# Optimization experiments

Measured on AMD Instinct MI355X. Metric: run time of the kernel, lower is better.

Reference implementation:

```python
import jax, jax.numpy as jnp
import numpy as np

N_H, N_O, D = 5000, 15000, 1024
E_HH, E_OO, E_HO = 20000, 40000, 40000


def setup_inputs() -> dict:
    key = jax.random.key(0)
    ks = jax.random.split(key, 20)
    N = N_H + N_O
    w = lambda k, shp: jax.random.normal(k, shp, dtype=jnp.float32) * 0.02
    inp = {
        'n_f': jax.random.normal(ks[0], (N, D), dtype=jnp.float32),
        'src_hh': jax.random.randint(ks[1], (E_HH,), 0, N_H),
        'dst_hh': jax.random.randint(ks[2], (E_HH,), 0, N_H),
        'src_oo': jax.random.randint(ks[3], (E_OO,), 0, N_O) + N_H,
        'dst_oo': jax.random.randint(ks[4], (E_OO,), 0, N_O) + N_H,
        'src_ho': jax.random.randint(ks[5], (E_HO,), 0, N_H),
        'dst_ho': jax.random.randint(ks[6], (E_HO,), 0, N_O) + N_H,
        'W_hh': w(ks[7], (2 * D, D)), 'b_hh': jnp.zeros((D,), jnp.float32),
        'W_oo': w(ks[8], (2 * D, D)), 'b_oo': jnp.zeros((D,), jnp.float32),
        'W_ho': w(ks[9], (2 * D, D)), 'b_ho': jnp.zeros((D,), jnp.float32),
        'W_att': w(ks[10], (D, 1)), 'b_att': jnp.zeros((1,), jnp.float32),
        'W_hn': w(ks[11], (2 * D, D)), 'b_hn': jnp.zeros((D,), jnp.float32),
        'W_on': w(ks[12], (2 * D, D)), 'b_on': jnp.zeros((D,), jnp.float32),
    }
    return inp


def reference(n_f, src_hh, dst_hh, src_oo, dst_oo, src_ho, dst_ho,
              W_hh, b_hh, W_oo, b_oo, W_ho, b_ho, W_att, b_att,
              W_hn, b_hn, W_on, b_on):
    N = n_f.shape[0]

    def edge_mlp(src, dst, W, b):
        # gather -> concat -> Linear -> ReLU  (H_H/O_O/H_O EdgeApplyModule)
        feat = jnp.concatenate([n_f[src], n_f[dst]], axis=1)  # [E, 2D]
        return jax.nn.relu(feat @ W + b)                       # [E, D]

    e_f = jnp.concatenate([
        edge_mlp(src_hh, dst_hh, W_hh, b_hh),
        edge_mlp(src_oo, dst_oo, W_oo, b_oo),
        edge_mlp(src_ho, dst_ho, W_ho, b_ho),
    ], axis=0)                                                 # [E, D]
    src = jnp.concatenate([src_hh, src_oo, src_ho])
    dst = jnp.concatenate([dst_hh, dst_oo, dst_ho])

    # E_AttentionModule: per-edge scalar attention logit
    a = (e_f @ W_att + b_att)[:, 0]                            # [E]

    # update_all: per-destination softmax over incoming edges (mailbox softmax)
    seg_max = jax.ops.segment_max(a, dst, num_segments=N)
    seg_max = jnp.where(jnp.isfinite(seg_max), seg_max, 0.0)
    ex = jnp.exp(a - seg_max[dst])
    denom = jax.ops.segment_sum(ex, dst, num_segments=N)
    alpha = ex / jnp.where(denom[dst] == 0, 1.0, denom[dst])   # [E]
    z = jax.ops.segment_sum(alpha[:, None] * n_f[src], dst, num_segments=N)  # [N, D]

    # Node apply: concat(n_f, z_f) -> Linear -> ReLU, separate h/o MLPs
    new_h = jax.nn.relu(jnp.concatenate([n_f[:N_H], z[:N_H]], axis=1) @ W_hn + b_hn)
    new_o = jax.nn.relu(jnp.concatenate([n_f[N_H:], z[N_H:]], axis=1) @ W_on + b_on)
    return jnp.concatenate([new_h, new_o], axis=0)             # [N, D] new_n_f
```

## Files before the change

kernel.cpp:

```cpp
#include <hip/hip_runtime.h>

#define N_H   5000
#define N_O   15000
#define N_TOT 20000
#define DD    1024
#define E_HH  20000
#define E_OO  40000
#define E_HO  40000
#define E_TOT 100000

typedef unsigned short u16;
typedef unsigned int u32;
typedef __attribute__((ext_vector_type(8))) short short8;
typedef __attribute__((ext_vector_type(4))) float f32x4;
typedef const __attribute__((address_space(1))) u32 gas_u32;
typedef __attribute__((address_space(3))) u32 las_u32;

__device__ __forceinline__ float bf2f(u16 u) {
    union { unsigned int i; float f; } v; v.i = ((unsigned int)u) << 16; return v.f;
}
__device__ __forceinline__ u16 f2bf(float f) {
    union { float f; unsigned int i; } v; v.f = f;
    unsigned int u = v.i;
    return (u16)((u + 0x7FFFu + ((u >> 16) & 1u)) >> 16);
}

#define CAST_NB 10000
#define CAT_NB  391
#define TW_NB   10240
struct TW  { const float* W; u16* dT; u16* dB; int ld; };
struct TW5 { TW t[5]; };
__global__ void cast_cat_tw(const float* __restrict__ in, u16* __restrict__ out,
                            const int* __restrict__ shh, const int* __restrict__ dhh,
                            const int* __restrict__ soo, const int* __restrict__ doo,
                            const int* __restrict__ sho, const int* __restrict__ dho,
                            int* __restrict__ src_all, int* __restrict__ dst_all,
                            int* __restrict__ deg, TW5 p) {
    __shared__ float tile[32][33];
    int b = blockIdx.x;
    if (b < CAST_NB) {
        size_t i = ((size_t)b * 256 + threadIdx.x) * 8;
        float4 a = *(const float4*)(in + i);
        float4 c = *(const float4*)(in + i + 4);
        u16 o[8] = {f2bf(a.x), f2bf(a.y), f2bf(a.z), f2bf(a.w),
                    f2bf(c.x), f2bf(c.y), f2bf(c.z), f2bf(c.w)};
        *(uint4*)(out + i) = *(const uint4*)o;
        return;
    }
    if (b < CAST_NB + CAT_NB) {
        int e = (b - CAST_NB) * 256 + threadIdx.x;
        if (e >= E_TOT) return;
        int s, d;
        if (e < E_HH)              { s = shh[e];               d = dhh[e]; }
        else if (e < E_HH + E_OO)  { s = soo[e - E_HH];        d = doo[e - E_HH]; }
        else                       { s = sho[e - E_HH - E_OO]; d = dho[e - E_HH - E_OO]; }
        src_all[e] = s; dst_all[e] = d;
        atomicAdd(&deg[d], 1);
        return;
    }
    int tb = b - CAST_NB - CAT_NB;
    int z = tb >> 10;
    int rem = tb & 1023;
    int bk = rem & 31, bn = rem >> 5;
    TW tw = p.t[z >> 1];
    int half = z & 1;
    int tx = threadIdx.x & 31, ty = threadIdx.x >> 5;
#pragma unroll
    for (int yy = 0; yy < 4; yy++) {
        int k = half * 1024 + bk * 32 + ty + yy * 8;
        int n = bn * 32 + tx;
        tile[ty + yy * 8][tx] = tw.W[(size_t)k * 1024 + n];
    }
    __syncthreads();
    u16* dst = half ? tw.dB : tw.dT;
#pragma unroll
    for (int yy = 0; yy < 4; yy++) {
        int n = bn * 32 + ty + yy * 8;
        int k = bk * 32 + tx;
        dst[(size_t)n * tw.ld + k] = f2bf(tile[tx][ty + yy * 8]);
    }
}

#define PROJ_NBM_H 40
#define PROJ_NBM_O 118
#define PROJ_NBN   24
__launch_bounds__(256)
__global__ void gemm_proj(const u16* __restrict__ Ah, const u16* __restrict__ Ao,
                          const u16* __restrict__ Bth, const u16* __restrict__ Bto,
                          u16* __restrict__ Ch, u16* __restrict__ Co) {
    __shared__ u16 smem[2][128][64];
    int bid = blockIdx.x;
    const u16* A; const u16* Bt; u16* C; int M;
    if (bid < PROJ_NBM_H * PROJ_NBN) { A = Ah; Bt = Bth; C = Ch; M = N_H; }
    else { bid -= PROJ_NBM_H * PROJ_NBN; A = Ao; Bt = Bto; C = Co; M = N_O; }
    int bm = bid / PROJ_NBN, bn = bid % PROJ_NBN;
    int t = threadIdx.x;
    int wave = t >> 6, lane = t & 63;
    int wr = wave >> 1, wc = wave & 1;
    int lm = lane & 15, q = lane >> 4;
    f32x4 acc[4][4] = {};
    int srow = lane >> 3;
    int scol = ((lane & 7) ^ srow) * 8;

    for (int k0 = 0; k0 < 1024; k0 += 64) {
#pragma unroll
        for (int it = 0; it < 4; it++) {
            int chunk = wave * 4 + it;
            int row = chunk * 8 + srow;
            int gr = bm * 128 + row; if (gr >= M) gr = M - 1;
            __builtin_amdgcn_global_load_lds((gas_u32*)(A + (size_t)gr * 1024 + k0 + scol),
                                             (las_u32*)&smem[0][chunk * 8][0], 16, 0, 0);
            __builtin_amdgcn_global_load_lds((gas_u32*)(Bt + (size_t)(bn * 128 + row) * 1024 + k0 + scol),
                                             (las_u32*)&smem[1][chunk * 8][0], 16, 0, 0);
        }
        __syncthreads();
#pragma unroll
        for (int ks = 0; ks < 64; ks += 32) {
            short8 af[4], bfr[4];
            int pc = (((ks >> 3) + q) ^ (lm & 7)) * 8;
#pragma unroll
            for (int i = 0; i < 4; i++)
                af[i] = *(const short8*)&smem[0][wr * 64 + i * 16 + lm][pc];
#pragma unroll
            for (int j = 0; j < 4; j++)
                bfr[j] = *(const short8*)&smem[1][wc * 64 + j * 16 + lm][pc];
#pragma unroll
            for (int i = 0; i < 4; i++)
#pragma unroll
                for (int j = 0; j < 4; j++)
                    acc[i][j] = __builtin_amdgcn_mfma_f32_16x16x32_bf16(af[i], bfr[j], acc[i][j], 0, 0, 0);
        }
        __syncthreads();
    }
    u16* sc = &smem[0][0][0];
#pragma unroll
    for (int i = 0; i < 4; i++)
#pragma unroll
        for (int j = 0; j < 4; j++)
#pragma unroll
            for (int r = 0; r < 4; r++)
                sc[(wr * 64 + i * 16 + q * 4 + r) * 128 + (wc * 64 + j * 16 + lm)] =
                    f2bf(acc[i][j][r]);
    __syncthreads();
#pragma unroll
    for (int it = 0; it < 8; it++) {
        int flat = it * 256 + t;
        int r = flat >> 4, cs = (flat & 15) * 8;
        int grow = bm * 128 + r;
        if (grow < M)
            *(uint4*)&C[(size_t)grow * 3072 + bn * 128 + cs] = *(const uint4*)&sc[r * 128 + cs];
    }
}

#define NODE_NBM_H 40
#define NODE_NBM_O 118
#define NODE_NBN   8
__launch_bounds__(256)
__global__ void gemm_node(const u16* __restrict__ nf_h, const u16* __restrict__ nf_o,
                          const u16* __restrict__ z_h, const u16* __restrict__ z_o,
                          const u16* __restrict__ Bthn, const u16* __restrict__ Bton,
                          const float* __restrict__ b_hn, const float* __restrict__ b_on,
                          float* __restrict__ out_h, float* __restrict__ out_o) {
    __shared__ u16 smem[2][128][64];
    int bid = (blockIdx.x & 7) * ((NODE_NBM_H + NODE_NBM_O) * NODE_NBN / 8)
            + (blockIdx.x >> 3);
    const u16 *A0, *A1, *Bt; const float* bias; float* C; int M;
    if (bid < NODE_NBM_H * NODE_NBN) {
        A0 = nf_h; A1 = z_h; Bt = Bthn; bias = b_hn; C = out_h; M = N_H;
    } else {
        bid -= NODE_NBM_H * NODE_NBN;
        A0 = nf_o; A1 = z_o; Bt = Bton; bias = b_on; C = out_o; M = N_O;
    }
    int bm = bid / NODE_NBN, bn = bid % NODE_NBN;
    int t = threadIdx.x;
    int wave = t >> 6, lane = t & 63;
    int wr = wave >> 1, wc = wave & 1;
    int lm = lane & 15, q = lane >> 4;
    f32x4 acc[4][4] = {};
    int srow = lane >> 3;
    int scol = ((lane & 7) ^ srow) * 8;

    for (int half = 0; half < 2; half++) {
        const u16* Asrc = half ? A1 : A0;
        const u16* Bth = Bt + half * 1024;
        for (int k0 = 0; k0 < 1024; k0 += 64) {
#pragma unroll
            for (int it = 0; it < 4; it++) {
                int chunk = wave * 4 + it;
                int row = chunk * 8 + srow;
                int gr = bm * 128 + row; if (gr >= M) gr = M - 1;
                __builtin_amdgcn_global_load_lds((gas_u32*)(Asrc + (size_t)gr * 1024 + k0 + scol),
                                                 (las_u32*)&smem[0][chunk * 8][0], 16, 0, 0);
                __builtin_amdgcn_global_load_lds((gas_u32*)(Bth + (size_t)(bn * 128 + row) * 2048 + k0 + scol),
                                                 (las_u32*)&smem[1][chunk * 8][0], 16, 0, 0);
            }
            __syncthreads();
#pragma unroll
            for (int ks = 0; ks < 64; ks += 32) {
                short8 af[4], bfr[4];
                int pc = (((ks >> 3) + q) ^ (lm & 7)) * 8;
#pragma unroll
                for (int i = 0; i < 4; i++)
                    af[i] = *(const short8*)&smem[0][wr * 64 + i * 16 + lm][pc];
#pragma unroll
                for (int j = 0; j < 4; j++)
                    bfr[j] = *(const short8*)&smem[1][wc * 64 + j * 16 + lm][pc];
#pragma unroll
                for (int i = 0; i < 4; i++)
#pragma unroll
                    for (int j = 0; j < 4; j++)
                        acc[i][j] = __builtin_amdgcn_mfma_f32_16x16x32_bf16(af[i], bfr[j], acc[i][j], 0, 0, 0);
            }
            __syncthreads();
        }
    }
    float* sf = (float*)&smem[0][0][0];
#pragma unroll
    for (int p = 0; p < 2; p++) {
        if (p) __syncthreads();
        if (wr == p) {
#pragma unroll
            for (int j = 0; j < 4; j++) {
                int col = wc * 64 + j * 16 + lm;
                float bv = bias[bn * 128 + col];
#pragma unroll
                for (int i = 0; i < 4; i++)
#pragma unroll
                    for (int r = 0; r < 4; r++)
                        sf[(i * 16 + q * 4 + r) * 128 + col] =
                            fmaxf(acc[i][j][r] + bv, 0.0f);
            }
        }
        __syncthreads();
#pragma unroll
        for (int it = 0; it < 8; it++) {
            int c = it * 256 + t;
            int rl = c >> 5, k4 = c & 31;
            int grow = bm * 128 + p * 64 + rl;
            if (grow < M)
                *(float4*)&C[(size_t)grow * 1024 + bn * 128 + k4 * 4] =
                    *(const float4*)&sf[rl * 128 + k4 * 4];
        }
    }
}

__global__ void edge_att(const u16* __restrict__ proj_h, const u16* __restrict__ proj_o,
                         const float* __restrict__ b_hh, const float* __restrict__ b_oo,
                         const float* __restrict__ b_ho,
                         const float* __restrict__ W_att, const float* __restrict__ b_att,
                         const int* __restrict__ src_all, const int* __restrict__ dst_all,
                         float* __restrict__ a_out) {
    int wave = threadIdx.x >> 6, lane = threadIdx.x & 63;
    int e0 = blockIdx.x * 64 + wave * 16;
    if (e0 >= E_TOT) return;
    const float* bsel = (e0 < E_HH) ? b_hh : (e0 < E_HH + E_OO ? b_oo : b_ho);
    float ww[16], bb[16];
#pragma unroll
    for (int i = 0; i < 16; i++) { ww[i] = W_att[lane * 16 + i]; bb[i] = bsel[lane * 16 + i]; }
    float batt = b_att[0];
    for (int k = 0; k < 16; k++) {
        int e = e0 + k;
        int s = src_all[e], d = dst_all[e];
        const u16 *u, *v;
        if (e < E_HH) {
            u = proj_h + (size_t)s * 3072;
            v = proj_h + (size_t)d * 3072 + 1024;
        } else if (e < E_HH + E_OO) {
            u = proj_o + (size_t)(s - N_H) * 3072;
            v = proj_o + (size_t)(d - N_H) * 3072 + 1024;
        } else {
            u = proj_h + (size_t)s * 3072 + 2048;
            v = proj_o + (size_t)(d - N_H) * 3072 + 2048;
        }
        int off = lane * 16;
        uint4 u0 = *(const uint4*)(u + off), u1 = *(const uint4*)(u + off + 8);
        uint4 v0 = *(const uint4*)(v + off), v1 = *(const uint4*)(v + off + 8);
        const u16* pu0 = (const u16*)&u0; const u16* pu1 = (const u16*)&u1;
        const u16* pv0 = (const u16*)&v0; const u16* pv1 = (const u16*)&v1;
        float acc = 0.f;
#pragma unroll
        for (int i = 0; i < 8; i++) {
            float tv = bf2f(pu0[i]) + bf2f(pv0[i]) + bb[i];
            acc += fmaxf(tv, 0.f) * ww[i];
        }
#pragma unroll
        for (int i = 0; i < 8; i++) {
            float tv = bf2f(pu1[i]) + bf2f(pv1[i]) + bb[8 + i];
            acc += fmaxf(tv, 0.f) * ww[8 + i];
        }
#pragma unroll
        for (int o = 32; o > 0; o >>= 1) acc += __shfl_down(acc, o);
        if (lane == 0) a_out[e] = acc + batt;
    }
}

__global__ void scan_deg(const int* __restrict__ deg, int* __restrict__ indptr) {
    __shared__ int sums[1024];
    int t = threadIdx.x;
    const int CH = 20;
    int beg = t * CH, end = beg + CH;
    if (end > N_TOT) end = N_TOT;
    if (beg > N_TOT) beg = N_TOT;
    int s = 0;
    for (int i = beg; i < end; i++) s += deg[i];
    sums[t] = s;
    __syncthreads();
    for (int off = 1; off < 1024; off <<= 1) {
        int v = sums[t];
        int add = (t >= off) ? sums[t - off] : 0;
        __syncthreads();
        sums[t] = v + add;
        __syncthreads();
    }
    int run = (t == 0) ? 0 : sums[t - 1];
    for (int i = beg; i < end; i++) { indptr[i] = run; run += deg[i]; }
    if (t == 1023) indptr[N_TOT] = sums[1023];
}

__global__ void fill_csr(const int* __restrict__ dst_all, const int* __restrict__ indptr,
                         int* __restrict__ cursor, int* __restrict__ edge_ids) {
    int e = blockIdx.x * 256 + threadIdx.x;
    if (e < E_TOT) {
        int d = dst_all[e];
        int pos = atomicAdd(&cursor[d], 1);
        edge_ids[indptr[d] + pos] = e;
    }
}

__launch_bounds__(256)
__global__ void soft_z_w(const float* __restrict__ a, const int* __restrict__ indptr,
                         const int* __restrict__ edge_ids, const int* __restrict__ src_all,
                         const u16* __restrict__ nf, u16* __restrict__ z) {
    int wave = threadIdx.x >> 6, lane = threadIdx.x & 63;
    int node = blockIdx.x * 4 + wave;
    if (node >= N_TOT) return;
    int beg = indptr[node];
    int deg = indptr[node + 1] - beg;
    float m = -1e30f, ssum = 0.f;
    for (int i = lane; i < deg; i += 64) {
        float av = a[edge_ids[beg + i]];
        if (av > m) { ssum *= __expf(m - av); m = av; }
        ssum += __expf(av - m);
    }
#pragma unroll
    for (int o = 32; o > 0; o >>= 1) {
        float m2 = __shfl_xor(m, o);
        float s2 = __shfl_xor(ssum, o);
        float mn = fmaxf(m, m2);
        ssum = ssum * __expf(m - mn) + s2 * __expf(m2 - mn);
        m = mn;
    }
    float inv = (ssum > 0.f) ? 1.0f / ssum : 0.f;
    float av16[16] = {};
    int base = lane * 16;
    for (int i = 0; i < deg; i++) {
        int eid = edge_ids[beg + i];
        float al = __expf(a[eid] - m) * inv;
        const u16* row = nf + (size_t)src_all[eid] * DD + base;
        uint4 p0 = *(const uint4*)row;
        uint4 p1 = *(const uint4*)(row + 8);
        const u16* pp0 = (const u16*)&p0;
        const u16* pp1 = (const u16*)&p1;
#pragma unroll
        for (int j = 0; j < 8; j++) av16[j]     += al * bf2f(pp0[j]);
#pragma unroll
        for (int j = 0; j < 8; j++) av16[8 + j] += al * bf2f(pp1[j]);
    }
    u16 ov[16];
#pragma unroll
    for (int j = 0; j < 16; j++) ov[j] = f2bf(av16[j]);
    const uint4* po = (const uint4*)ov;
    *(uint4*)(z + (size_t)node * DD + base)     = po[0];
    *(uint4*)(z + (size_t)node * DD + base + 8) = po[1];
}

extern "C" void kernel_launch(void* const* d_in, const int* in_sizes, int n_in,
                              void* d_out, int out_size, void* d_ws, size_t ws_size,
                              hipStream_t stream) {
    const float* nf   = (const float*)d_in[0];
    const int* shh    = (const int*)d_in[1];
    const int* dhh    = (const int*)d_in[2];
    const int* soo    = (const int*)d_in[3];
    const int* doo    = (const int*)d_in[4];
    const int* sho    = (const int*)d_in[5];
    const int* dho    = (const int*)d_in[6];
    const float* W_hh = (const float*)d_in[7];
    const float* b_hh = (const float*)d_in[8];
    const float* W_oo = (const float*)d_in[9];
    const float* b_oo = (const float*)d_in[10];
    const float* W_ho = (const float*)d_in[11];
    const float* b_ho = (const float*)d_in[12];
    const float* W_att= (const float*)d_in[13];
    const float* b_att= (const float*)d_in[14];
    const float* W_hn = (const float*)d_in[15];
    const float* b_hn = (const float*)d_in[16];
    const float* W_on = (const float*)d_in[17];
    const float* b_on = (const float*)d_in[18];
    float* out = (float*)d_out;

    char* ws = (char*)d_ws;
    size_t off = 0;
    auto alloc = [&](size_t bytes) -> char* {
        char* p = ws + off;
        off += (bytes + 255) & ~(size_t)255;
        return p;
    };
    u16* nf_bf = (u16*)alloc((size_t)N_TOT * DD * 2);
    u16* Bt_h  = (u16*)alloc((size_t)3072 * 1024 * 2);
    u16* Bt_o  = (u16*)alloc((size_t)3072 * 1024 * 2);
    u16* Bt_hn = (u16*)alloc((size_t)1024 * 2048 * 2);
    u16* Bt_on = (u16*)alloc((size_t)1024 * 2048 * 2);
    u16* proj_h = (u16*)alloc((size_t)N_H * 3072 * 2);
    u16* proj_o = (u16*)alloc((size_t)N_O * 3072 * 2);
    u16* z_bf   = proj_h;
    float* a_log  = (float*)alloc(E_TOT * 4);
    int* src_all  = (int*)alloc(E_TOT * 4);
    int* dst_all  = (int*)alloc(E_TOT * 4);
    int* deg      = (int*)alloc(2 * N_TOT * 4);
    int* cursor   = deg + N_TOT;
    int* indptr   = (int*)alloc((N_TOT + 1) * 4);
    int* edge_ids = (int*)alloc(E_TOT * 4);
    (void)ws_size; (void)in_sizes; (void)n_in; (void)out_size;

    hipMemsetAsync(deg, 0, 2 * N_TOT * 4, stream);
    TW5 tws;
    tws.t[0] = {W_hh, Bt_h,                       Bt_h + (size_t)1024 * 1024, 1024};
    tws.t[1] = {W_oo, Bt_o,                       Bt_o + (size_t)1024 * 1024, 1024};
    tws.t[2] = {W_ho, Bt_h + (size_t)2048 * 1024, Bt_o + (size_t)2048 * 1024, 1024};
    tws.t[3] = {W_hn, Bt_hn,                      Bt_hn + 1024,               2048};
    tws.t[4] = {W_on, Bt_on,                      Bt_on + 1024,               2048};
    cast_cat_tw<<<CAST_NB + CAT_NB + TW_NB, 256, 0, stream>>>(
        nf, nf_bf, shh, dhh, soo, doo, sho, dho, src_all, dst_all, deg, tws);

    const u16* nf_bf_o = nf_bf + (size_t)N_H * DD;
    gemm_proj<<<(PROJ_NBM_H + PROJ_NBM_O) * PROJ_NBN, 256, 0, stream>>>(
        nf_bf, nf_bf_o, Bt_h, Bt_o, proj_h, proj_o);

    edge_att<<<(E_TOT + 63) / 64, 256, 0, stream>>>(proj_h, proj_o, b_hh, b_oo, b_ho,
                                                    W_att, b_att, src_all, dst_all, a_log);

    scan_deg<<<1, 1024, 0, stream>>>(deg, indptr);
    fill_csr<<<(E_TOT + 255) / 256, 256, 0, stream>>>(dst_all, indptr, cursor, edge_ids);

    soft_z_w<<<N_TOT / 4, 256, 0, stream>>>(a_log, indptr, edge_ids, src_all, nf_bf, z_bf);

    gemm_node<<<(NODE_NBM_H + NODE_NBM_O) * NODE_NBN, 256, 0, stream>>>(
        nf_bf, nf_bf_o, z_bf, z_bf + (size_t)N_H * DD, Bt_hn, Bt_on,
        b_hn, b_on, out, out + (size_t)N_H * DD);
}
```

Measured before the change: 579.1 us.

## Build CSR via single-block LDS histogram scan and fuse fill into projection GEMM

Removes the memset and global atomic degree counting and replaces them with a single-block kernel that histograms destinations into shared memory in two halves, scans them, and writes indptr plus an initialized cursor. The CSR fill step is appended as extra blocks of the projection GEMM launch, so it overlaps with the GEMM and saves two launches. The cost is a serial single-block kernel that reads all 100k edges twice, now sitting on the critical path before the GEMM.

```diff
diff --git a/kernel.cpp b/kernel.cpp
--- a/kernel.cpp
+++ b/kernel.cpp
@@ -35,7 +35,7 @@
                             const int* __restrict__ soo, const int* __restrict__ doo,
                             const int* __restrict__ sho, const int* __restrict__ dho,
                             int* __restrict__ src_all, int* __restrict__ dst_all,
-                            int* __restrict__ deg, TW5 p) {
+                            TW5 p) {
     __shared__ float tile[32][33];
     int b = blockIdx.x;
     if (b < CAST_NB) {
@@ -55,7 +55,6 @@
         else if (e < E_HH + E_OO)  { s = soo[e - E_HH];        d = doo[e - E_HH]; }
         else                       { s = sho[e - E_HH - E_OO]; d = dho[e - E_HH - E_OO]; }
         src_all[e] = s; dst_all[e] = d;
-        atomicAdd(&deg[d], 1);
         return;
     }
     int tb = b - CAST_NB - CAT_NB;
@@ -81,15 +80,72 @@
     }
 }
 
+__launch_bounds__(1024)
+__global__ void scan_count(const int* __restrict__ dst_all, int* __restrict__ indptr,
+                           int* __restrict__ cursor) {
+    __shared__ int cnt[10000];
+    __shared__ int sums[1024];
+    int t = threadIdx.x;
+    int total = 0;
+    for (int half = 0; half < 2; half++) {
+        int lo = half * 10000;
+        for (int i = t; i < 10000; i += 1024) cnt[i] = 0;
+        __syncthreads();
+        for (int e = t; e < E_TOT; e += 1024) {
+            u32 d = (u32)(dst_all[e] - lo);
+            if (d < 10000u) atomicAdd(&cnt[d], 1);
+        }
+        __syncthreads();
+        const int CH = 10;
+        int beg = t * CH;
+        int s = 0;
+        if (beg < 10000)
+            for (int i = 0; i < CH; i++) s += cnt[beg + i];
+        sums[t] = s;
+        __syncthreads();
+        for (int off2 = 1; off2 < 1024; off2 <<= 1) {
+            int v = sums[t];
+            int add = (t >= off2) ? sums[t - off2] : 0;
+            __syncthreads();
+            sums[t] = v + add;
+            __syncthreads();
+        }
+        if (beg < 10000) {
+            int run = total + (t == 0 ? 0 : sums[t - 1]);
+            for (int i = 0; i < CH; i++) {
+                indptr[lo + beg + i] = run;
+                cursor[lo + beg + i] = run;
+                run += cnt[beg + i];
+            }
+        }
+        __syncthreads();
+        total += sums[1023];
+        __syncthreads();
+    }
+    if (t == 0) indptr[N_TOT] = total;
+}
+
 #define PROJ_NBM_H 40
 #define PROJ_NBM_O 118
 #define PROJ_NBN   24
+#define PROJ_GEMM_NB ((PROJ_NBM_H + PROJ_NBM_O) * PROJ_NBN)
+#define FILL_NB 391
 __launch_bounds__(256)
 __global__ void gemm_proj(const u16* __restrict__ Ah, const u16* __restrict__ Ao,
                           const u16* __restrict__ Bth, const u16* __restrict__ Bto,
-                          u16* __restrict__ Ch, u16* __restrict__ Co) {
+                          u16* __restrict__ Ch, u16* __restrict__ Co,
+                          const int* __restrict__ dst_all, int* __restrict__ cursor,
+                          int* __restrict__ edge_ids) {
     __shared__ u16 smem[2][128][64];
     int bid = blockIdx.x;
+    if (bid >= PROJ_GEMM_NB) {
+        int e = (bid - PROJ_GEMM_NB) * 256 + threadIdx.x;
+        if (e < E_TOT) {
+            int pos = atomicAdd(&cursor[dst_all[e]], 1);
+            edge_ids[pos] = e;
+        }
+        return;
+    }
     const u16* A; const u16* Bt; u16* C; int M;
     if (bid < PROJ_NBM_H * PROJ_NBN) { A = Ah; Bt = Bth; C = Ch; M = N_H; }
     else { bid -= PROJ_NBM_H * PROJ_NBN; A = Ao; Bt = Bto; C = Co; M = N_O; }
@@ -291,39 +347,6 @@
 #pragma unroll
         for (int o = 32; o > 0; o >>= 1) acc += __shfl_down(acc, o);
         if (lane == 0) a_out[e] = acc + batt;
-    }
-}
-
-__global__ void scan_deg(const int* __restrict__ deg, int* __restrict__ indptr) {
-    __shared__ int sums[1024];
-    int t = threadIdx.x;
-    const int CH = 20;
-    int beg = t * CH, end = beg + CH;
-    if (end > N_TOT) end = N_TOT;
-    if (beg > N_TOT) beg = N_TOT;
-    int s = 0;
-    for (int i = beg; i < end; i++) s += deg[i];
-    sums[t] = s;
-    __syncthreads();
-    for (int off = 1; off < 1024; off <<= 1) {
-        int v = sums[t];
-        int add = (t >= off) ? sums[t - off] : 0;
-        __syncthreads();
-        sums[t] = v + add;
-        __syncthreads();
-    }
-    int run = (t == 0) ? 0 : sums[t - 1];
-    for (int i = beg; i < end; i++) { indptr[i] = run; run += deg[i]; }
-    if (t == 1023) indptr[N_TOT] = sums[1023];
-}
-
-__global__ void fill_csr(const int* __restrict__ dst_all, const int* __restrict__ indptr,
-                         int* __restrict__ cursor, int* __restrict__ edge_ids) {
-    int e = blockIdx.x * 256 + threadIdx.x;
-    if (e < E_TOT) {
-        int d = dst_all[e];
-        int pos = atomicAdd(&cursor[d], 1);
-        edge_ids[indptr[d] + pos] = e;
     }
 }
 
@@ -422,7 +445,6 @@
     int* edge_ids = (int*)alloc(E_TOT * 4);
     (void)ws_size; (void)in_sizes; (void)n_in; (void)out_size;
 
-    hipMemsetAsync(deg, 0, 2 * N_TOT * 4, stream);
     TW5 tws;
     tws.t[0] = {W_hh, Bt_h,                       Bt_h + (size_t)1024 * 1024, 1024};
     tws.t[1] = {W_oo, Bt_o,                       Bt_o + (size_t)1024 * 1024, 1024};
@@ -430,17 +452,16 @@
     tws.t[3] = {W_hn, Bt_hn,                      Bt_hn + 1024,               2048};
     tws.t[4] = {W_on, Bt_on,                      Bt_on + 1024,               2048};
     cast_cat_tw<<<CAST_NB + CAT_NB + TW_NB, 256, 0, stream>>>(
-        nf, nf_bf, shh, dhh, soo, doo, sho, dho, src_all, dst_all, deg, tws);
+        nf, nf_bf, shh, dhh, soo, doo, sho, dho, src_all, dst_all, tws);
+
+    scan_count<<<1, 1024, 0, stream>>>(dst_all, indptr, cursor);
 
     const u16* nf_bf_o = nf_bf + (size_t)N_H * DD;
-    gemm_proj<<<(PROJ_NBM_H + PROJ_NBM_O) * PROJ_NBN, 256, 0, stream>>>(
-        nf_bf, nf_bf_o, Bt_h, Bt_o, proj_h, proj_o);
+    gemm_proj<<<PROJ_GEMM_NB + FILL_NB, 256, 0, stream>>>(
+        nf_bf, nf_bf_o, Bt_h, Bt_o, proj_h, proj_o, dst_all, cursor, edge_ids);
 
     edge_att<<<(E_TOT + 63) / 64, 256, 0, stream>>>(proj_h, proj_o, b_hh, b_oo, b_ho,
                                                     W_att, b_att, src_all, dst_all, a_log);
-
-    scan_deg<<<1, 1024, 0, stream>>>(deg, indptr);
-    fill_csr<<<(E_TOT + 255) / 256, 256, 0, stream>>>(dst_all, indptr, cursor, edge_ids);
 
     soft_z_w<<<N_TOT / 4, 256, 0, stream>>>(a_log, indptr, edge_ids, src_all, nf_bf, z_bf);
 
```

Measured after the change: 605.3 us. 1.05x slower.
